# Kernel tuning notes

Hardware: AMD Instinct MI355X
Metric: run time of the kernel (lower is better)

Reference implementation:

```python
import jax, jax.numpy as jnp
import numpy as np

N_CODES = 4096
D = 256


def setup_inputs() -> dict:
    key = jax.random.key(0)
    k_v, k_w = jax.random.split(key)
    v = jax.random.normal(k_v, (8, 2048, D), dtype=jnp.float32)
    # Embedding init ~ N(0,1), then softmax over dim=1, then row 0 set to 1/d (empty feature)
    w = jax.random.normal(k_w, (N_CODES, D), dtype=jnp.float32)
    w = jax.nn.softmax(w, axis=1)
    w = w.at[0].set(1.0 / D)
    return {"v": v, "vectors": w}


def reference(v, vectors):
    n, d = vectors.shape
    cb = vectors[1:]  # exclude the fixed empty feature at index 0
    # ||v - c||^2 = ||v||^2 - 2 v.c + ||c||^2  (avoids [..., n, d] intermediate)
    v2 = jnp.sum(v * v, axis=-1, keepdims=True)              # [..., 1]
    c2 = jnp.sum(cb * cb, axis=-1)                           # [n-1]
    diff = v2 - 2.0 * jnp.einsum('...d,nd->...n', v, cb) + c2  # [..., n-1]
    idx = jnp.argmin(diff, axis=-1) + 1                      # [...]
    # empty-feature mask: any component differs from 1/d
    mask = jnp.any(v != (1.0 / d), axis=-1)
    idx = jnp.where(mask, idx, 0)
    out = vectors[idx]                                       # gather == onehot @ vectors
    loss = jnp.mean(jnp.square(out - jax.lax.stop_gradient(v)))
    used = jnp.array(0, dtype=jnp.int32)  # eval mode: usage pool is empty
    return out, idx, loss, used
```

## Files before the change

### kernel.cpp

```cpp
#include <hip/hip_runtime.h>
#include <hip/hip_fp16.h>
#include <math.h>
#include <stdint.h>


#define M_TOTAL 16384
#define NCODES  4096
#define D_DIM   256

#define OUT_OFF_IDX  (M_TOTAL * D_DIM)
#define OUT_OFF_LOSS (OUT_OFF_IDX + M_TOTAL)

#define NPART 32
#define VPLANE (M_TOTAL * D_DIM)

typedef _Float16 half8 __attribute__((ext_vector_type(8)));
typedef float    float16v __attribute__((ext_vector_type(16)));

__global__ __launch_bounds__(256) void prep_v_kernel(
    const float* __restrict__ X, _Float16* __restrict__ hi, _Float16* __restrict__ lo,
    float* __restrict__ sq)
{
  __shared__ float T[16 * 264];
  const int t = threadIdx.x;
  const int rloc = t >> 4, seg = t & 15;
  const int row = blockIdx.x * 16 + rloc;
  const float* src = X + (size_t)row * D_DIM + seg * 16;
  float4 x[4];
#pragma unroll
  for (int u = 0; u < 4; ++u) x[u] = ((const float4*)src)[u];
  union { half8 v; _Float16 e[8]; } uh[2], ul[2];
#pragma unroll
  for (int u = 0; u < 4; ++u) {
    float e4[4] = {x[u].x, x[u].y, x[u].z, x[u].w};
#pragma unroll
    for (int j = 0; j < 4; ++j) {
      const int e = u * 4 + j;
      float s = e4[j] * 1024.0f;
      _Float16 h = (_Float16)s;
      uh[e >> 3].e[e & 7] = h;
      ul[e >> 3].e[e & 7] = (_Float16)(s - (float)h);
    }
    *(float4*)&T[rloc * 264 + seg * 16 + u * 4] = x[u];
  }
  _Float16* hd = hi + (size_t)row * D_DIM + seg * 16;
  _Float16* ld = lo + (size_t)row * D_DIM + seg * 16;
  *(half8*)hd = uh[0].v; *(half8*)(hd + 8) = uh[1].v;
  *(half8*)ld = ul[0].v; *(half8*)(ld + 8) = ul[1].v;
  __syncthreads();
  const int half = (t >> 3) & 1, j = t & 7;
  const float* tr = &T[rloc * 264 + half * 128 + j];
  float r = __fmul_rn(tr[0], tr[0]);
#pragma unroll
  for (int i = 1; i < 16; ++i) { float e = tr[8 * i]; r = __fadd_rn(r, __fmul_rn(e, e)); }
  r = __fadd_rn(r, __shfl_xor(r, 1));
  r = __fadd_rn(r, __shfl_xor(r, 2));
  r = __fadd_rn(r, __shfl_xor(r, 4));
  r = __fadd_rn(r, __shfl_xor(r, 8));
  if ((t & 15) == 0) sq[row] = r;
}

__global__ __launch_bounds__(256) void prep_w_kernel(
    const float* __restrict__ W, _Float16* __restrict__ Bp, float* __restrict__ c2)
{
  __shared__ float T[16 * 264];
  const int t = threadIdx.x;
  const int rloc = t >> 4, seg = t & 15;
  const int row = blockIdx.x * 16 + rloc;
  const float* src = W + (size_t)row * D_DIM + seg * 16;
  float4 x[4];
#pragma unroll
  for (int u = 0; u < 4; ++u) x[u] = ((const float4*)src)[u];
  union { half8 v; _Float16 e[8]; } uh[2], ul[2];
#pragma unroll
  for (int u = 0; u < 4; ++u) {
    float e4[4] = {x[u].x, x[u].y, x[u].z, x[u].w};
#pragma unroll
    for (int j = 0; j < 4; ++j) {
      const int e = u * 4 + j;
      float s = e4[j] * 1024.0f;
      _Float16 h = (_Float16)s;
      uh[e >> 3].e[e & 7] = h;
      ul[e >> 3].e[e & 7] = (_Float16)(s - (float)h);
    }
    *(float4*)&T[rloc * 264 + seg * 16 + u * 4] = x[u];
  }
  const int panel = row >> 5, nin = row & 31;
  _Float16* dst = Bp + ((size_t)panel * 16 + seg) * 2048 + nin * 8;
#pragma unroll
  for (int lh = 0; lh < 2; ++lh) {
    *(half8*)(dst + lh * 256)        = uh[lh].v;
    *(half8*)(dst + 1024 + lh * 256) = ul[lh].v;
  }
  __syncthreads();
  const int half = (t >> 3) & 1, j = t & 7;
  const float* tr = &T[rloc * 264 + half * 128 + j];
  float r = __fmul_rn(tr[0], tr[0]);
#pragma unroll
  for (int i = 1; i < 16; ++i) { float e = tr[8 * i]; r = __fadd_rn(r, __fmul_rn(e, e)); }
  r = __fadd_rn(r, __shfl_xor(r, 1));
  r = __fadd_rn(r, __shfl_xor(r, 2));
  r = __fadd_rn(r, __shfl_xor(r, 4));
  r = __fadd_rn(r, __shfl_xor(r, 8));
  if ((t & 15) == 0) c2[row] = r;
}

__global__ __launch_bounds__(256, 2) void vq_mfma_kernel(
    const _Float16* __restrict__ Vhi, const _Float16* __restrict__ Vlo,
    const _Float16* __restrict__ Bp,
    const float* __restrict__ v2, const float* __restrict__ c2,
    uint64_t* __restrict__ pk)
{
  __shared__ __align__(16) char smem_raw[37888];
  _Float16* As = (_Float16*)smem_raw;
  uint64_t* red2 = (uint64_t*)(smem_raw + 33792);

  const int tid  = threadIdx.x;
  const int lane = tid & 63;
  const int wave = tid >> 6;
  const int wr = wave >> 1, wc = wave & 1;
  const int l31 = lane & 31, lhi = lane >> 5;

  const int bid = blockIdx.x;
  const int panel = (bid & 7) * 4 + ((bid >> 3) & 3);
  const int mblk  = bid >> 5;
  const int m0 = mblk * 256;
  const int n0 = panel * 128;
  const int p32 = panel * 4 + wc * 2;

  int src[4], dst[4];
#pragma unroll
  for (int u = 0; u < 4; ++u) {
    const int g = tid + 256 * u, m = g >> 2, kb = g & 3;
    src[u] = (m0 + m) * D_DIM + kb * 8;
    dst[u] = m * 32 + (kb ^ (m & 3)) * 8;
  }

  float16v acc[4][2];
#pragma unroll
  for (int mb = 0; mb < 4; ++mb)
#pragma unroll
    for (int nb = 0; nb < 2; ++nb) acc[mb][nb] = (float16v)0.0f;

  half8 sh[4], sl[4];
#pragma unroll
  for (int u = 0; u < 4; ++u) {
    sh[u] = *(const half8*)(Vhi + src[u]);
    sl[u] = *(const half8*)(Vlo + src[u]);
  }

  half8 bh[2][2], bl[2][2];
#pragma unroll
  for (int nb = 0; nb < 2; ++nb) {
    const _Float16* bp = Bp + ((size_t)(p32 + nb) * 16) * 2048 + lane * 8;
    bh[0][nb] = *(const half8*)bp;
    bl[0][nb] = *(const half8*)(bp + 1024);
  }

  for (int kt = 0; kt < 8; ++kt) {
    if (kt) __syncthreads();
#pragma unroll
    for (int u = 0; u < 4; ++u) {
      *(half8*)(As + dst[u])        = sh[u];
      *(half8*)(As + 8192 + dst[u]) = sl[u];
    }
    __syncthreads();
    if (kt < 7) {
#pragma unroll
      for (int u = 0; u < 4; ++u) {
        sh[u] = *(const half8*)(Vhi + src[u] + (kt + 1) * 32);
        sl[u] = *(const half8*)(Vlo + src[u] + (kt + 1) * 32);
      }
    }
#pragma unroll
    for (int ks = 0; ks < 2; ++ks) {
      const int kstep = kt * 2 + ks;
      const int cur = kstep & 1, nxt = cur ^ 1;
      if (kstep < 15) {
#pragma unroll
        for (int nb = 0; nb < 2; ++nb) {
          const _Float16* bp = Bp + ((size_t)(p32 + nb) * 16 + kstep + 1) * 2048 + lane * 8;
          bh[nxt][nb] = *(const half8*)bp;
          bl[nxt][nb] = *(const half8*)(bp + 1024);
        }
      }
      half8 ah[4], al[4];
#pragma unroll
      for (int mb = 0; mb < 4; ++mb) {
        const int m = wr * 128 + mb * 32 + l31;
        const int c = (ks * 2 + lhi) ^ (m & 3);
        ah[mb] = *(const half8*)(As + m * 32 + c * 8);
        al[mb] = *(const half8*)(As + 8192 + m * 32 + c * 8);
      }
#pragma unroll
      for (int nb = 0; nb < 2; ++nb)
#pragma unroll
        for (int mb = 0; mb < 4; ++mb)
          acc[mb][nb] = __builtin_amdgcn_mfma_f32_32x32x16_f16(ah[mb], bh[cur][nb], acc[mb][nb], 0, 0, 0);
#pragma unroll
      for (int nb = 0; nb < 2; ++nb)
#pragma unroll
        for (int mb = 0; mb < 4; ++mb)
          acc[mb][nb] = __builtin_amdgcn_mfma_f32_32x32x16_f16(ah[mb], bl[cur][nb], acc[mb][nb], 0, 0, 0);
#pragma unroll
      for (int nb = 0; nb < 2; ++nb)
#pragma unroll
        for (int mb = 0; mb < 4; ++mb)
          acc[mb][nb] = __builtin_amdgcn_mfma_f32_32x32x16_f16(al[mb], bh[cur][nb], acc[mb][nb], 0, 0, 0);
    }
  }

  float c2r[2];
#pragma unroll
  for (int nb = 0; nb < 2; ++nb) c2r[nb] = c2[n0 + wc * 64 + nb * 32 + l31];

  __syncthreads();
  uint64_t* wbuf = (uint64_t*)smem_raw + wave * 1056;

#pragma unroll
  for (int mb = 0; mb < 4; ++mb) {
#pragma unroll
    for (int r = 0; r < 16; ++r) {
      const int rowin = (r & 3) + 8 * (r >> 2) + 4 * lhi;
      const float v2m = v2[m0 + wr * 128 + mb * 32 + rowin];
      uint64_t b = ~0ULL;
#pragma unroll
      for (int nb = 0; nb < 2; ++nb) {
        const int n = n0 + wc * 64 + nb * 32 + l31;
        float dot = acc[mb][nb][r] * 0x1p-20f;
        float dd  = __fadd_rn(__fsub_rn(v2m, 2.0f * dot), c2r[nb]);
        if (n == 0) dd = INFINITY;
        uint64_t p = ((uint64_t)__float_as_uint(dd) << 32) | (uint32_t)n;
        if (p < b) b = p;
      }
      wbuf[(r * 2 + lhi) * 33 + l31] = b;
    }
    __syncthreads();
    {
      const int f = lane >> 1, hf = lane & 1;
      const uint64_t* rp = wbuf + f * 33 + hf * 16;
      uint64_t m = rp[0];
#pragma unroll
      for (int i = 1; i < 16; ++i) { uint64_t v = rp[i]; if (v < m) m = v; }
      uint64_t o = __shfl_xor((unsigned long long)m, 1);
      if (o < m) m = o;
      if (hf == 0) {
        const int r_ = f >> 1, lh2 = f & 1;
        const int rowin = (r_ & 3) + 8 * (r_ >> 2) + 4 * lh2;
        red2[(wr * 128 + mb * 32 + rowin) * 2 + wc] = m;
      }
    }
    __syncthreads();
  }

  uint64_t a0 = red2[tid * 2], a1 = red2[tid * 2 + 1];
  pk[(size_t)panel * M_TOTAL + m0 + tid] = a0 < a1 ? a0 : a1;
}

__global__ __launch_bounds__(256) void gather_kernel(
    const float* __restrict__ V, const float* __restrict__ W,
    const uint64_t* __restrict__ pk,
    float* __restrict__ out, float* __restrict__ outIdx,
    float* __restrict__ lossPartial)
{
  const int q = blockIdx.x * 4 + (threadIdx.x >> 6);
  const int l = threadIdx.x & 63;
  uint64_t b = (l < NPART) ? pk[(size_t)l * M_TOTAL + q] : ~0ULL;
#pragma unroll
  for (int off = 32; off; off >>= 1) {
    uint64_t o = __shfl_xor((unsigned long long)b, off);
    if (o < b) b = o;
  }
  float4 vv = *(const float4*)(V + (size_t)q * D_DIM + l * 4);
  const float inv = 0.00390625f;
  bool ne = (vv.x != inv) | (vv.y != inv) | (vv.z != inv) | (vv.w != inv);
  const int idx = __ballot(ne) ? (int)(uint32_t)b : 0;
  float4 o4 = *(const float4*)(W + (size_t)idx * D_DIM + l * 4);
  *(float4*)(out + (size_t)q * D_DIM + l * 4) = o4;
  if (l == 0) outIdx[q] = (float)idx;
  float dx = o4.x - vv.x, dy = o4.y - vv.y, dz = o4.z - vv.z, dw = o4.w - vv.w;
  float s = dx * dx + dy * dy + dz * dz + dw * dw;
#pragma unroll
  for (int off = 32; off; off >>= 1) s += __shfl_xor(s, off);
  if (l == 0) lossPartial[q] = s;
}

__global__ __launch_bounds__(256) void finalize_kernel(
    const float* __restrict__ lossPartial, float* __restrict__ out)
{
  const int t = threadIdx.x;
  __shared__ float red[256];
  float s = 0.0f;
  for (int i = t; i < M_TOTAL; i += 256) s += lossPartial[i];
  red[t] = s;
  __syncthreads();
  for (int st = 128; st > 0; st >>= 1) {
    if (t < st) red[t] += red[t + st];
    __syncthreads();
  }
  if (t == 0) {
    out[0] = (float)((double)red[0] / (double)(M_TOTAL * D_DIM));
    out[1] = 0.0f;
  }
}

extern "C" void kernel_launch(void* const* d_in, const int* in_sizes, int n_in,
                              void* d_out, int out_size, void* d_ws, size_t ws_size,
                              hipStream_t stream) {
  const float* V = (const float*)d_in[0];
  const float* W = (const float*)d_in[1];
  float* out = (float*)d_out;

  _Float16* Vhi = (_Float16*)d_out;
  _Float16* Vlo = Vhi + VPLANE;

  char* ws = (char*)d_ws;
  _Float16* Bp  = (_Float16*)(ws);
  float*    c2  = (float*)(ws + 8388608);
  float*    v2  = (float*)(ws + 8388608 + 16384);
  uint64_t* pk  = (uint64_t*)(ws + 8388608 + 16384 + 65536);
  float* lossPartial = (float*)(ws + 8388608 + 16384 + 65536 + 4194304);

  prep_w_kernel<<<NCODES / 16, 256, 0, stream>>>(W, Bp, c2);
  prep_v_kernel<<<M_TOTAL / 16, 256, 0, stream>>>(V, Vhi, Vlo, v2);
  vq_mfma_kernel<<<2048, 256, 0, stream>>>(Vhi, Vlo, Bp, v2, c2, pk);
  gather_kernel<<<M_TOTAL / 4, 256, 0, stream>>>(V, W, pk, out, out + OUT_OFF_IDX, lossPartial);
  finalize_kernel<<<1, 256, 0, stream>>>(lossPartial, out + OUT_OFF_LOSS);
}
```

Baseline: 212.8 us.

## Double-buffer A tile in LDS, merge prep kernels, reduce argmin with atomicMin

Fuses the codebook and input prep kernels into one launch, which also initialises the packed argmin buffer. The MFMA kernel now double-buffers the A tile in shared memory, so one barrier per k-tile replaces two and LDS stores overlap with compute. Per-panel partial minima are replaced by 64-bit atomicMin into a single buffer, removing the 32-way reduction read in the gather kernel. This raises shared memory use per block and adds atomic traffic.

```diff
diff --git a/kernel.cpp b/kernel.cpp
--- a/kernel.cpp
+++ b/kernel.cpp
@@ -11,20 +11,27 @@
 #define OUT_OFF_IDX  (M_TOTAL * D_DIM)
 #define OUT_OFF_LOSS (OUT_OFF_IDX + M_TOTAL)
 
-#define NPART 32
 #define VPLANE (M_TOTAL * D_DIM)
 
 typedef _Float16 half8 __attribute__((ext_vector_type(8)));
 typedef float    float16v __attribute__((ext_vector_type(16)));
 
-__global__ __launch_bounds__(256) void prep_v_kernel(
-    const float* __restrict__ X, _Float16* __restrict__ hi, _Float16* __restrict__ lo,
-    float* __restrict__ sq)
+__global__ __launch_bounds__(256) void prep_kernel(
+    const float* __restrict__ V, const float* __restrict__ W,
+    _Float16* __restrict__ Vhi, _Float16* __restrict__ Vlo,
+    _Float16* __restrict__ Bp, float* __restrict__ v2, float* __restrict__ c2,
+    uint64_t* __restrict__ pk)
 {
   __shared__ float T[16 * 264];
   const int t = threadIdx.x;
   const int rloc = t >> 4, seg = t & 15;
-  const int row = blockIdx.x * 16 + rloc;
+  const bool isW = blockIdx.x < 256;
+  const int bid2 = isW ? blockIdx.x : (blockIdx.x - 256);
+  const int row = bid2 * 16 + rloc;
+  const float* X = isW ? W : V;
+
+  if (!isW && bid2 < 64) pk[bid2 * 256 + t] = ~0ULL;
+
   const float* src = X + (size_t)row * D_DIM + seg * 16;
   float4 x[4];
 #pragma unroll
@@ -43,10 +50,20 @@
     }
     *(float4*)&T[rloc * 264 + seg * 16 + u * 4] = x[u];
   }
-  _Float16* hd = hi + (size_t)row * D_DIM + seg * 16;
-  _Float16* ld = lo + (size_t)row * D_DIM + seg * 16;
-  *(half8*)hd = uh[0].v; *(half8*)(hd + 8) = uh[1].v;
-  *(half8*)ld = ul[0].v; *(half8*)(ld + 8) = ul[1].v;
+  if (isW) {
+    const int panel = row >> 5, nin = row & 31;
+    _Float16* dst = Bp + ((size_t)panel * 16 + seg) * 2048 + nin * 8;
+#pragma unroll
+    for (int lh = 0; lh < 2; ++lh) {
+      *(half8*)(dst + lh * 256)        = uh[lh].v;
+      *(half8*)(dst + 1024 + lh * 256) = ul[lh].v;
+    }
+  } else {
+    _Float16* hd = Vhi + (size_t)row * D_DIM + seg * 16;
+    _Float16* ld = Vlo + (size_t)row * D_DIM + seg * 16;
+    *(half8*)hd = uh[0].v; *(half8*)(hd + 8) = uh[1].v;
+    *(half8*)ld = ul[0].v; *(half8*)(ld + 8) = ul[1].v;
+  }
   __syncthreads();
   const int half = (t >> 3) & 1, j = t & 7;
   const float* tr = &T[rloc * 264 + half * 128 + j];
@@ -57,52 +74,7 @@
   r = __fadd_rn(r, __shfl_xor(r, 2));
   r = __fadd_rn(r, __shfl_xor(r, 4));
   r = __fadd_rn(r, __shfl_xor(r, 8));
-  if ((t & 15) == 0) sq[row] = r;
-}
-
-__global__ __launch_bounds__(256) void prep_w_kernel(
-    const float* __restrict__ W, _Float16* __restrict__ Bp, float* __restrict__ c2)
-{
-  __shared__ float T[16 * 264];
-  const int t = threadIdx.x;
-  const int rloc = t >> 4, seg = t & 15;
-  const int row = blockIdx.x * 16 + rloc;
-  const float* src = W + (size_t)row * D_DIM + seg * 16;
-  float4 x[4];
-#pragma unroll
-  for (int u = 0; u < 4; ++u) x[u] = ((const float4*)src)[u];
-  union { half8 v; _Float16 e[8]; } uh[2], ul[2];
-#pragma unroll
-  for (int u = 0; u < 4; ++u) {
-    float e4[4] = {x[u].x, x[u].y, x[u].z, x[u].w};
-#pragma unroll
-    for (int j = 0; j < 4; ++j) {
-      const int e = u * 4 + j;
-      float s = e4[j] * 1024.0f;
-      _Float16 h = (_Float16)s;
-      uh[e >> 3].e[e & 7] = h;
-      ul[e >> 3].e[e & 7] = (_Float16)(s - (float)h);
-    }
-    *(float4*)&T[rloc * 264 + seg * 16 + u * 4] = x[u];
-  }
-  const int panel = row >> 5, nin = row & 31;
-  _Float16* dst = Bp + ((size_t)panel * 16 + seg) * 2048 + nin * 8;
-#pragma unroll
-  for (int lh = 0; lh < 2; ++lh) {
-    *(half8*)(dst + lh * 256)        = uh[lh].v;
-    *(half8*)(dst + 1024 + lh * 256) = ul[lh].v;
-  }
-  __syncthreads();
-  const int half = (t >> 3) & 1, j = t & 7;
-  const float* tr = &T[rloc * 264 + half * 128 + j];
-  float r = __fmul_rn(tr[0], tr[0]);
-#pragma unroll
-  for (int i = 1; i < 16; ++i) { float e = tr[8 * i]; r = __fadd_rn(r, __fmul_rn(e, e)); }
-  r = __fadd_rn(r, __shfl_xor(r, 1));
-  r = __fadd_rn(r, __shfl_xor(r, 2));
-  r = __fadd_rn(r, __shfl_xor(r, 4));
-  r = __fadd_rn(r, __shfl_xor(r, 8));
-  if ((t & 15) == 0) c2[row] = r;
+  if ((t & 15) == 0) { if (isW) c2[row] = r; else v2[row] = r; }
 }
 
 __global__ __launch_bounds__(256, 2) void vq_mfma_kernel(
@@ -111,9 +83,9 @@
     const float* __restrict__ v2, const float* __restrict__ c2,
     uint64_t* __restrict__ pk)
 {
-  __shared__ __align__(16) char smem_raw[37888];
+  __shared__ __align__(16) char smem_raw[69632];
   _Float16* As = (_Float16*)smem_raw;
-  uint64_t* red2 = (uint64_t*)(smem_raw + 33792);
+  uint64_t* red2 = (uint64_t*)(smem_raw + 65536);
 
   const int tid  = threadIdx.x;
   const int lane = tid & 63;
@@ -148,6 +120,11 @@
     sh[u] = *(const half8*)(Vhi + src[u]);
     sl[u] = *(const half8*)(Vlo + src[u]);
   }
+#pragma unroll
+  for (int u = 0; u < 4; ++u) {
+    *(half8*)(As + dst[u])        = sh[u];
+    *(half8*)(As + 8192 + dst[u]) = sl[u];
+  }
 
   half8 bh[2][2], bl[2][2];
 #pragma unroll
@@ -156,15 +133,11 @@
     bh[0][nb] = *(const half8*)bp;
     bl[0][nb] = *(const half8*)(bp + 1024);
   }
+  __syncthreads();
 
   for (int kt = 0; kt < 8; ++kt) {
-    if (kt) __syncthreads();
-#pragma unroll
-    for (int u = 0; u < 4; ++u) {
-      *(half8*)(As + dst[u])        = sh[u];
-      *(half8*)(As + 8192 + dst[u]) = sl[u];
-    }
-    __syncthreads();
+    const int cur = kt & 1;
+    _Float16* Ac = As + cur * 16384;
     if (kt < 7) {
 #pragma unroll
       for (int u = 0; u < 4; ++u) {
@@ -175,13 +148,13 @@
 #pragma unroll
     for (int ks = 0; ks < 2; ++ks) {
       const int kstep = kt * 2 + ks;
-      const int cur = kstep & 1, nxt = cur ^ 1;
+      const int pcur = kstep & 1, pnxt = pcur ^ 1;
       if (kstep < 15) {
 #pragma unroll
         for (int nb = 0; nb < 2; ++nb) {
           const _Float16* bp = Bp + ((size_t)(p32 + nb) * 16 + kstep + 1) * 2048 + lane * 8;
-          bh[nxt][nb] = *(const half8*)bp;
-          bl[nxt][nb] = *(const half8*)(bp + 1024);
+          bh[pnxt][nb] = *(const half8*)bp;
+          bl[pnxt][nb] = *(const half8*)(bp + 1024);
         }
       }
       half8 ah[4], al[4];
@@ -189,32 +162,40 @@
       for (int mb = 0; mb < 4; ++mb) {
         const int m = wr * 128 + mb * 32 + l31;
         const int c = (ks * 2 + lhi) ^ (m & 3);
-        ah[mb] = *(const half8*)(As + m * 32 + c * 8);
-        al[mb] = *(const half8*)(As + 8192 + m * 32 + c * 8);
+        ah[mb] = *(const half8*)(Ac + m * 32 + c * 8);
+        al[mb] = *(const half8*)(Ac + 8192 + m * 32 + c * 8);
       }
 #pragma unroll
       for (int nb = 0; nb < 2; ++nb)
 #pragma unroll
         for (int mb = 0; mb < 4; ++mb)
-          acc[mb][nb] = __builtin_amdgcn_mfma_f32_32x32x16_f16(ah[mb], bh[cur][nb], acc[mb][nb], 0, 0, 0);
+          acc[mb][nb] = __builtin_amdgcn_mfma_f32_32x32x16_f16(ah[mb], bh[pcur][nb], acc[mb][nb], 0, 0, 0);
 #pragma unroll
       for (int nb = 0; nb < 2; ++nb)
 #pragma unroll
         for (int mb = 0; mb < 4; ++mb)
-          acc[mb][nb] = __builtin_amdgcn_mfma_f32_32x32x16_f16(ah[mb], bl[cur][nb], acc[mb][nb], 0, 0, 0);
+          acc[mb][nb] = __builtin_amdgcn_mfma_f32_32x32x16_f16(ah[mb], bl[pcur][nb], acc[mb][nb], 0, 0, 0);
 #pragma unroll
       for (int nb = 0; nb < 2; ++nb)
 #pragma unroll
         for (int mb = 0; mb < 4; ++mb)
-          acc[mb][nb] = __builtin_amdgcn_mfma_f32_32x32x16_f16(al[mb], bh[cur][nb], acc[mb][nb], 0, 0, 0);
-    }
+          acc[mb][nb] = __builtin_amdgcn_mfma_f32_32x32x16_f16(al[mb], bh[pcur][nb], acc[mb][nb], 0, 0, 0);
+    }
+    if (kt < 7) {
+      _Float16* An = As + (cur ^ 1) * 16384;
+#pragma unroll
+      for (int u = 0; u < 4; ++u) {
+        *(half8*)(An + dst[u])        = sh[u];
+        *(half8*)(An + 8192 + dst[u]) = sl[u];
+      }
+    }
+    __syncthreads();
   }
 
   float c2r[2];
 #pragma unroll
   for (int nb = 0; nb < 2; ++nb) c2r[nb] = c2[n0 + wc * 64 + nb * 32 + l31];
 
-  __syncthreads();
   uint64_t* wbuf = (uint64_t*)smem_raw + wave * 1056;
 
 #pragma unroll
@@ -254,7 +235,7 @@
   }
 
   uint64_t a0 = red2[tid * 2], a1 = red2[tid * 2 + 1];
-  pk[(size_t)panel * M_TOTAL + m0 + tid] = a0 < a1 ? a0 : a1;
+  atomicMin((unsigned long long*)&pk[m0 + tid], (unsigned long long)(a0 < a1 ? a0 : a1));
 }
 
 __global__ __launch_bounds__(256) void gather_kernel(
@@ -265,12 +246,7 @@
 {
   const int q = blockIdx.x * 4 + (threadIdx.x >> 6);
   const int l = threadIdx.x & 63;
-  uint64_t b = (l < NPART) ? pk[(size_t)l * M_TOTAL + q] : ~0ULL;
-#pragma unroll
-  for (int off = 32; off; off >>= 1) {
-    uint64_t o = __shfl_xor((unsigned long long)b, off);
-    if (o < b) b = o;
-  }
+  const uint64_t b = pk[q];
   float4 vv = *(const float4*)(V + (size_t)q * D_DIM + l * 4);
   const float inv = 0.00390625f;
   bool ne = (vv.x != inv) | (vv.y != inv) | (vv.z != inv) | (vv.w != inv);
@@ -319,10 +295,9 @@
   float*    c2  = (float*)(ws + 8388608);
   float*    v2  = (float*)(ws + 8388608 + 16384);
   uint64_t* pk  = (uint64_t*)(ws + 8388608 + 16384 + 65536);
-  float* lossPartial = (float*)(ws + 8388608 + 16384 + 65536 + 4194304);
-
-  prep_w_kernel<<<NCODES / 16, 256, 0, stream>>>(W, Bp, c2);
-  prep_v_kernel<<<M_TOTAL / 16, 256, 0, stream>>>(V, Vhi, Vlo, v2);
+  float* lossPartial = (float*)(ws + 8388608 + 16384 + 65536 + 131072);
+
+  prep_kernel<<<1280, 256, 0, stream>>>(V, W, Vhi, Vlo, Bp, v2, c2, pk);
   vq_mfma_kernel<<<2048, 256, 0, stream>>>(Vhi, Vlo, Bp, v2, c2, pk);
   gather_kernel<<<M_TOTAL / 4, 256, 0, stream>>>(V, W, pk, out, out + OUT_OFF_IDX, lossPartial);
   finalize_kernel<<<1, 256, 0, stream>>>(lossPartial, out + OUT_OFF_LOSS);
```

New measurement: 204.3 us. 4.0% less time.
